# Kernel tuning notes

Hardware: AMD Instinct MI355X
Metric: run time of the kernel (lower is better)

Reference implementation:

```python
import jax, jax.numpy as jnp
import numpy as np

H, W = 250, 400
N_RAYS = H * W          # 100000 (one patch)
N_SAMPLES = 1_000_000
P, C, DIM = 50000, 16, 8
STEP_SIZE = 0.005
DENSITY_SHIFT = 0.0
DENSITY_SCALE = min(1.0 / (1.0 - DENSITY_SHIFT), 25.0)


def setup_inputs() -> dict:
    key = jax.random.key(0)
    ks = jax.random.split(key, 12)
    return {
        "trivecs": jax.random.normal(ks[0], (P, C, 3, DIM), dtype=jnp.float32),
        "densities": jax.random.normal(ks[1], (P, C), dtype=jnp.float32),
        "colors": jax.random.normal(ks[2], (P, C, 3), dtype=jnp.float32),
        "local_gweight_s": jax.random.uniform(ks[3], (N_SAMPLES, 3), dtype=jnp.float32),
        "local_gweight_l": jax.random.uniform(ks[4], (N_SAMPLES, 3), dtype=jnp.float32),
        "t_min": jax.random.uniform(ks[5], (N_RAYS,), dtype=jnp.float32),
        "bg": jax.random.uniform(ks[6], (3,), dtype=jnp.float32),
        "local_gindx_s": jax.random.randint(ks[7], (N_SAMPLES, 3), 0, DIM, dtype=jnp.int32),
        "local_gindx_l": jax.random.randint(ks[8], (N_SAMPLES, 3), 0, DIM, dtype=jnp.int32),
        "tensoRF_id": jax.random.randint(ks[9], (N_SAMPLES,), 0, P, dtype=jnp.int32),
        "ray_id": jnp.sort(jax.random.randint(ks[10], (N_SAMPLES,), 0, N_RAYS, dtype=jnp.int32)),
        "step_id": jax.random.randint(ks[11], (N_SAMPLES,), 0, 200, dtype=jnp.int32),
    }


def reference(trivecs, densities, colors, local_gweight_s, local_gweight_l,
              t_min, bg, local_gindx_s, local_gindx_l, tensoRF_id, ray_id, step_id):
    # --- compute_feature: trilinear tensor-decomposition gather ---
    def interp(a):
        vs = trivecs[tensoRF_id, :, a, local_gindx_s[:, a]]  # [N, C]
        vl = trivecs[tensoRF_id, :, a, local_gindx_l[:, a]]  # [N, C]
        return vs * local_gweight_s[:, a:a + 1] + vl * local_gweight_l[:, a:a + 1]

    feature = interp(0) * interp(1) * interp(2)               # [N, C]
    sigma = (feature * densities[tensoRF_id]).sum(axis=1)     # [N]
    color = jnp.einsum('nc,nck->nk', feature, colors[tensoRF_id])  # [N, 3]

    # --- density activation & alpha ---
    density = jax.nn.softplus(sigma - DENSITY_SHIFT * 10.0) * DENSITY_SCALE
    alpha = 1.0 - jnp.exp(-density * STEP_SIZE)               # [N]

    # --- Alphas2Weights: per-ray exclusive transmittance (ray_id sorted) ---
    log_t = -density * STEP_SIZE                              # == log(1 - alpha)
    seg_total = jax.ops.segment_sum(log_t, ray_id, num_segments=N_RAYS)  # [R]
    seg_offset = jnp.concatenate([jnp.zeros((1,), log_t.dtype),
                                  jnp.cumsum(seg_total)[:-1]])           # [R]
    excl = jnp.cumsum(log_t) - log_t - seg_offset[ray_id]     # within-segment excl cumsum
    weights = alpha * jnp.exp(excl)                           # [N]
    bg_weight = jnp.exp(seg_total)                            # [R], prod(1-alpha) per ray

    # --- ray compositing ---
    rgb = jax.nn.sigmoid(color)                               # [N, 3]
    rgb_map = jax.ops.segment_sum(weights[:, None] * rgb, ray_id, num_segments=N_RAYS)
    rgb_map = rgb_map + bg_weight[:, None] * bg[None, :]
    z_val = t_min[ray_id] + step_id.astype(jnp.float32) * STEP_SIZE
    depth_map = jax.ops.segment_sum(weights * z_val, ray_id, num_segments=N_RAYS)
    alpha_map = 1.0 - bg_weight

    rgb_map = rgb_map.T.reshape(3, H, W)
    depth_map = depth_map.reshape(H, W)
    alpha_map = alpha_map.reshape(H, W)
    return rgb_map, depth_map, alpha_map
```

## Files before the change

### kernel.cpp

```cpp
#include <hip/hip_runtime.h>
#include <math.h>

#define HN       250
#define WN       400
#define N_RAYS   (HN * WN)
#define N_SAMP   1000000
#define P_TENSO  50000
#define STEP_SZ  0.005f
#define DENS_SCALE 1.0f
#define NB_SCAN  ((P_TENSO + 1023) / 1024)


#define OFF_PACK    0
#define OFF_RESULTS 32000000
#define OFF_PERM    48000000
#define OFF_IPERM   52000000
#define OFF_RANK    56000000
#define OFF_CURSOR  60000000
#define OFF_STARTS  60200000
#define OFF_BSUMS   60400000
#define OFF_FLAG    60400512
#define OFF_RSTART  60401024
#define WS_NEED     (60401024 + 400004 + 64)

#define ROW_STRIDE 20
#define TV_F   (24 * ROW_STRIDE)
#define SLAB_F (TV_F + 16 + 48)

__global__ __launch_bounds__(256) void pack_bounds_rank(
    const int*   __restrict__ tenso_id,
    const int*   __restrict__ ray_id,
    const int*   __restrict__ gis, const int* __restrict__ gil,
    const float* __restrict__ gws, const float* __restrict__ gwl,
    int* __restrict__ cursor,
    int* __restrict__ rank,
    int* __restrict__ ray_start,
    float4* __restrict__ pack)
{
    int n = blockIdx.x * 256 + threadIdx.x;
    if (n >= N_SAMP) return;

    const int tid = tenso_id[n];
    rank[n] = atomicAdd(&cursor[tid], 1);

    unsigned bits = (unsigned)gis[n*3+0] | ((unsigned)gis[n*3+1] << 3) | ((unsigned)gis[n*3+2] << 6)
                  | ((unsigned)gil[n*3+0] << 9) | ((unsigned)gil[n*3+1] << 12) | ((unsigned)gil[n*3+2] << 15);
    float4 A = make_float4(gws[n*3+0], gws[n*3+1], gws[n*3+2], gwl[n*3+0]);
    float4 B = make_float4(gwl[n*3+1], gwl[n*3+2], __uint_as_float(bits), 0.0f);
    pack[(size_t)n * 2 + 0] = A;
    pack[(size_t)n * 2 + 1] = B;

    int r = ray_id[n];
    int rprev = (n == 0) ? -1 : ray_id[n - 1];
    for (int q = rprev + 1; q <= r; ++q) ray_start[q] = n;
    if (n == N_SAMP - 1) {
        for (int q = r + 1; q <= N_RAYS; ++q) ray_start[q] = N_SAMP;
    }
}

__global__ __launch_bounds__(256) void scan_fused(
    const int* __restrict__ cursor,
    int* __restrict__ starts,
    int* __restrict__ bsums,
    int* __restrict__ flag)
{
    __shared__ int lds[257];
    const int b = blockIdx.x;
    const int t = threadIdx.x;
    const int base = b * 1024 + t * 4;

    int v[4]; int s = 0;
    #pragma unroll
    for (int i = 0; i < 4; ++i) {
        int idx = base + i;
        v[i] = (idx < P_TENSO) ? cursor[idx] : 0;
        s += v[i];
    }
    lds[t] = s;
    __syncthreads();
    for (int d = 1; d < 256; d <<= 1) {
        int x = (t >= d) ? lds[t - d] : 0;
        __syncthreads();
        lds[t] += x;
        __syncthreads();
    }
    if (t == 255) bsums[b] = lds[255];

    __threadfence();
    __syncthreads();
    if (t == 0) {
        atomicAdd(flag, 1);
        while (atomicAdd(flag, 0) < gridDim.x) { }
    }
    __syncthreads();
    __threadfence();

    if (t < 64) {
        int x = (t < b) ? bsums[t] : 0;
        #pragma unroll
        for (int m = 1; m < 64; m <<= 1) x += __shfl_xor(x, m);
        if (t == 0) lds[256] = x;
    }
    __syncthreads();
    const int pre = lds[256];

    int run = pre + ((t > 0) ? lds[t - 1] : 0);
    #pragma unroll
    for (int i = 0; i < 4; ++i) {
        int idx = base + i;
        if (idx < P_TENSO) starts[idx] = run;
        run += v[i];
    }
}

__global__ __launch_bounds__(256) void finalize_perm(
    const int* __restrict__ tenso_id,
    const int* __restrict__ rank,
    const int* __restrict__ starts,
    int* __restrict__ perm,
    int* __restrict__ iperm)
{
    int n = blockIdx.x * 256 + threadIdx.x;
    if (n >= N_SAMP) return;
    int pos = starts[tenso_id[n]] + rank[n];
    iperm[n] = pos;
    perm[pos] = n;
}

__global__ __launch_bounds__(256) void gather_phase(
    const float* __restrict__ trivecs,
    const float* __restrict__ densities,
    const float* __restrict__ colors,
    const int*   __restrict__ starts,
    const int*   __restrict__ counts,
    const int*   __restrict__ perm,
    const float4* __restrict__ pack,
    float* __restrict__ results_f)
{
    __shared__ __align__(16) float lds[4 * SLAB_F];
    const int lane = threadIdx.x & 63;
    const int wv   = threadIdx.x >> 6;
    const int t    = blockIdx.x * 4 + wv;
    if (t >= P_TENSO) return;

    const int start = starts[t];
    const int cnt   = counts[t];
    if (cnt == 0) return;

    float* slab = lds + wv * SLAB_F;
    float* dl   = slab + TV_F;
    float* cl   = dl + 16;

    const float* tvg = trivecs + (size_t)t * 384;
    #pragma unroll
    for (int i = 0; i < 6; ++i) {
        int l = lane + i * 64;
        int c = l / 24;
        int rem = l - c * 24;
        slab[rem * ROW_STRIDE + c] = tvg[l];
    }
    if (lane < 16) dl[lane] = densities[(size_t)t * 16 + lane];
    if (lane < 48) {
        int c = lane / 3, k = lane - c * 3;
        cl[k * 16 + c] = colors[(size_t)t * 48 + lane];
    }

    const int g = lane >> 2;
    const int j = lane & 3;

    const float4 dens4 = *(const float4*)(dl + 4 * j);
    const float4 col0  = *(const float4*)(cl + 4 * j);
    const float4 col1  = *(const float4*)(cl + 16 + 4 * j);
    const float4 col2  = *(const float4*)(cl + 32 + 4 * j);

    const int end = start + cnt;
    const int niter = (cnt + 15) >> 4;

    for (int it = 0; it < niter; ++it) {
        const int pos = start + it * 16 + g;
        const bool valid = (pos < end);
        const int cp = valid ? pos : (end - 1);
        const int n = perm[cp];
        const float4 A = pack[(size_t)n * 2 + 0];
        const float4 B = pack[(size_t)n * 2 + 1];
        const unsigned bits = __float_as_uint(B.z);

        float4 f;
        {
            const int is = bits & 7, il = (bits >> 9) & 7;
            const float4 vs = *(const float4*)(slab + is * ROW_STRIDE + 4 * j);
            const float4 vl = *(const float4*)(slab + il * ROW_STRIDE + 4 * j);
            f.x = vs.x * A.x + vl.x * A.w;
            f.y = vs.y * A.x + vl.y * A.w;
            f.z = vs.z * A.x + vl.z * A.w;
            f.w = vs.w * A.x + vl.w * A.w;
        }
        {
            const int is = (bits >> 3) & 7, il = (bits >> 12) & 7;
            const float4 vs = *(const float4*)(slab + (8 + is) * ROW_STRIDE + 4 * j);
            const float4 vl = *(const float4*)(slab + (8 + il) * ROW_STRIDE + 4 * j);
            f.x *= vs.x * A.y + vl.x * B.x;
            f.y *= vs.y * A.y + vl.y * B.x;
            f.z *= vs.z * A.y + vl.z * B.x;
            f.w *= vs.w * A.y + vl.w * B.x;
        }
        {
            const int is = (bits >> 6) & 7, il = (bits >> 15) & 7;
            const float4 vs = *(const float4*)(slab + (16 + is) * ROW_STRIDE + 4 * j);
            const float4 vl = *(const float4*)(slab + (16 + il) * ROW_STRIDE + 4 * j);
            f.x *= vs.x * A.z + vl.x * B.y;
            f.y *= vs.y * A.z + vl.y * B.y;
            f.z *= vs.z * A.z + vl.z * B.y;
            f.w *= vs.w * A.z + vl.w * B.y;
        }

        float s0 = f.x * dens4.x + f.y * dens4.y + f.z * dens4.z + f.w * dens4.w;
        float s1 = f.x * col0.x  + f.y * col0.y  + f.z * col0.z  + f.w * col0.w;
        float s2 = f.x * col1.x  + f.y * col1.y  + f.z * col1.z  + f.w * col1.w;
        float s3 = f.x * col2.x  + f.y * col2.y  + f.z * col2.z  + f.w * col2.w;

        s0 += __shfl_xor(s0, 1); s0 += __shfl_xor(s0, 2);
        s1 += __shfl_xor(s1, 1); s1 += __shfl_xor(s1, 2);
        s2 += __shfl_xor(s2, 1); s2 += __shfl_xor(s2, 2);
        s3 += __shfl_xor(s3, 1); s3 += __shfl_xor(s3, 2);

        const float sj = (j == 0) ? s0 : (j == 1) ? s1 : (j == 2) ? s2 : s3;
        float val;
        if (j == 0) {
            float dens = fmaxf(sj, 0.0f) + __logf(1.0f + __expf(-fabsf(sj)));
            val = -(dens * DENS_SCALE) * STEP_SZ;
        } else {
            val = 1.0f / (1.0f + __expf(-sj));
        }
        if (valid) results_f[(size_t)pos * 4 + j] = val;
    }
}

__global__ __launch_bounds__(256) void ray_render(
    const float4* __restrict__ results,
    const int*    __restrict__ iperm,
    const float*  __restrict__ t_min,
    const float*  __restrict__ bg,
    const int*    __restrict__ ray_start,
    const int*    __restrict__ step_id,
    float* __restrict__ out)
{
    int r = blockIdx.x * 256 + threadIdx.x;
    if (r >= N_RAYS) return;
    const int s = ray_start[r];
    const int e = ray_start[r + 1];
    const float tmin_r = t_min[r];

    float T = 0.0f, aR = 0.0f, aG = 0.0f, aB = 0.0f, aD = 0.0f;
    for (int n = s; n < e; ++n) {
        const int pos = iperm[n];
        float4 res = results[pos];
        const float lt = res.x;
        const float w = (1.0f - __expf(lt)) * __expf(T);
        T += lt;
        const float z = tmin_r + (float)step_id[n] * STEP_SZ;
        aR += w * res.y;
        aG += w * res.z;
        aB += w * res.w;
        aD += w * z;
    }
    const float bgw = __expf(T);
    out[0 * N_RAYS + r] = aR + bgw * bg[0];
    out[1 * N_RAYS + r] = aG + bgw * bg[1];
    out[2 * N_RAYS + r] = aB + bgw * bg[2];
    out[3 * N_RAYS + r] = aD;
    out[4 * N_RAYS + r] = 1.0f - bgw;
}

__global__ __launch_bounds__(256) void trivec_render_fallback(
    const float* __restrict__ trivecs, const float* __restrict__ densities,
    const float* __restrict__ colors, const float* __restrict__ gws,
    const float* __restrict__ gwl, const float* __restrict__ t_min,
    const float* __restrict__ bg, const int* __restrict__ gis,
    const int* __restrict__ gil, const int* __restrict__ tenso_id,
    const int* __restrict__ ray_id, const int* __restrict__ step_id,
    float* __restrict__ out)
{
    const int lane = threadIdx.x & 63;
    const int r = blockIdx.x * 4 + (threadIdx.x >> 6);
    if (r >= N_RAYS) return;
    const int c = lane & 15;
    const int g = lane >> 4;
    int lo = 0, hi = N_SAMP;
    while (lo < hi) { int mid = (lo + hi) >> 1; if (ray_id[mid] < r) lo = mid + 1; else hi = mid; }
    const int seg_start = lo;
    hi = N_SAMP;
    while (lo < hi) { int mid = (lo + hi) >> 1; if (ray_id[mid] < r + 1) lo = mid + 1; else hi = mid; }
    const int seg_end = lo;
    const float tmin_r = t_min[r];
    float Tlog = 0.0f, accR = 0.0f, accG = 0.0f, accB = 0.0f, accD = 0.0f;
    const int niter = (seg_end - seg_start + 3) >> 2;
    for (int it = 0; it < niter; ++it) {
        const int n = seg_start + it * 4 + g;
        const bool valid = (n < seg_end);
        const int nc = valid ? n : (seg_end - 1);
        const int tid = tenso_id[nc];
        const float* tv = trivecs + (size_t)tid * 384 + c * 24;
        float f = 1.0f;
        #pragma unroll
        for (int a = 0; a < 3; ++a) {
            const int is = gis[nc*3+a], il = gil[nc*3+a];
            const float wS = gws[nc*3+a], wL = gwl[nc*3+a];
            f *= (tv[a*8+is] * wS + tv[a*8+il] * wL);
        }
        const float dns = densities[(size_t)tid * 16 + c];
        const float* colp = colors + ((size_t)tid * 16 + c) * 3;
        float s0 = f*dns, s1 = f*colp[0], s2 = f*colp[1], s3 = f*colp[2];
        #pragma unroll
        for (int m = 1; m < 16; m <<= 1) {
            s0 += __shfl_xor(s0, m); s1 += __shfl_xor(s1, m);
            s2 += __shfl_xor(s2, m); s3 += __shfl_xor(s3, m);
        }
        float dens = fmaxf(s0, 0.0f) + __logf(1.0f + __expf(-fabsf(s0)));
        const float lt = valid ? (-dens * STEP_SZ) : 0.0f;
        const float alpha = 1.0f - __expf(lt);
        const float rr = 1.0f/(1.0f+__expf(-s1)), gg = 1.0f/(1.0f+__expf(-s2)), bb = 1.0f/(1.0f+__expf(-s3));
        const float z = tmin_r + (float)step_id[nc] * STEP_SZ;
        const float lt0 = __shfl(lt,0), lt1 = __shfl(lt,16), lt2 = __shfl(lt,32), lt3 = __shfl(lt,48);
        float excl = Tlog;
        if (g > 0) excl += lt0;
        if (g > 1) excl += lt1;
        if (g > 2) excl += lt2;
        const float w = alpha * __expf(excl);
        Tlog += lt0 + lt1 + lt2 + lt3;
        accR += w*rr; accG += w*gg; accB += w*bb; accD += w*z;
    }
    accR += __shfl_xor(accR,16); accR += __shfl_xor(accR,32);
    accG += __shfl_xor(accG,16); accG += __shfl_xor(accG,32);
    accB += __shfl_xor(accB,16); accB += __shfl_xor(accB,32);
    accD += __shfl_xor(accD,16); accD += __shfl_xor(accD,32);
    const float bgw = __expf(Tlog);
    if (lane == 0) {
        out[0*N_RAYS+r] = accR + bgw*bg[0];
        out[1*N_RAYS+r] = accG + bgw*bg[1];
        out[2*N_RAYS+r] = accB + bgw*bg[2];
        out[3*N_RAYS+r] = accD;
        out[4*N_RAYS+r] = 1.0f - bgw;
    }
}

extern "C" void kernel_launch(void* const* d_in, const int* in_sizes, int n_in,
                              void* d_out, int out_size, void* d_ws, size_t ws_size,
                              hipStream_t stream) {
    const float* trivecs   = (const float*)d_in[0];
    const float* densities = (const float*)d_in[1];
    const float* colors    = (const float*)d_in[2];
    const float* gws       = (const float*)d_in[3];
    const float* gwl       = (const float*)d_in[4];
    const float* t_min     = (const float*)d_in[5];
    const float* bg        = (const float*)d_in[6];
    const int*   gis       = (const int*)d_in[7];
    const int*   gil       = (const int*)d_in[8];
    const int*   tenso_id  = (const int*)d_in[9];
    const int*   ray_id    = (const int*)d_in[10];
    const int*   step_id   = (const int*)d_in[11];
    float* out = (float*)d_out;

    if (ws_size < (size_t)WS_NEED) {
        trivec_render_fallback<<<(N_RAYS + 3) / 4, 256, 0, stream>>>(
            trivecs, densities, colors, gws, gwl, t_min, bg,
            gis, gil, tenso_id, ray_id, step_id, out);
        return;
    }

    char* ws = (char*)d_ws;
    float4* pack     = (float4*)(ws + OFF_PACK);
    float4* results  = (float4*)(ws + OFF_RESULTS);
    int*    perm     = (int*)(ws + OFF_PERM);
    int*    iperm    = (int*)(ws + OFF_IPERM);
    int*    rank     = (int*)(ws + OFF_RANK);
    int*    cursor   = (int*)(ws + OFF_CURSOR);
    int*    starts   = (int*)(ws + OFF_STARTS);
    int*    bsums    = (int*)(ws + OFF_BSUMS);
    int*    flag     = (int*)(ws + OFF_FLAG);
    int*    raystart = (int*)(ws + OFF_RSTART);

    hipMemsetAsync(ws + OFF_CURSOR, 0, (OFF_FLAG + 64) - OFF_CURSOR, stream);

    pack_bounds_rank<<<(N_SAMP + 255) / 256, 256, 0, stream>>>(
        tenso_id, ray_id, gis, gil, gws, gwl, cursor, rank, raystart, pack);
    scan_fused<<<NB_SCAN, 256, 0, stream>>>(cursor, starts, bsums, flag);
    finalize_perm<<<(N_SAMP + 255) / 256, 256, 0, stream>>>(
        tenso_id, rank, starts, perm, iperm);
    gather_phase<<<(P_TENSO + 3) / 4, 256, 0, stream>>>(
        trivecs, densities, colors, starts, cursor, perm, pack, (float*)results);
    ray_render<<<(N_RAYS + 255) / 256, 256, 0, stream>>>(
        results, iperm, t_min, bg, raystart, step_id, out);
}
```

Baseline: 283.2 us.

## Scatter packed sample data into tensor-sorted order and write results in sample order

The per-sample packed weights and indices are now scattered directly into tensoRF-sorted order, with the original sample index stored in the spare fourth lane. The gather kernel then reads them contiguously instead of going through a perm indirection. It writes results back at the original sample index, so ray_render reads results sequentially without iperm. This drops the perm/iperm arrays and their random reads, at the cost of a scattered 32-byte write in build_sorted and scattered 16-byte result writes in the gather.

```diff
diff --git a/kernel.cpp b/kernel.cpp
--- a/kernel.cpp
+++ b/kernel.cpp
@@ -11,44 +11,31 @@
 #define NB_SCAN  ((P_TENSO + 1023) / 1024)
 
 
-#define OFF_PACK    0
+#define OFF_SORT    0
 #define OFF_RESULTS 32000000
-#define OFF_PERM    48000000
-#define OFF_IPERM   52000000
-#define OFF_RANK    56000000
-#define OFF_CURSOR  60000000
-#define OFF_STARTS  60200000
-#define OFF_BSUMS   60400000
-#define OFF_FLAG    60400512
-#define OFF_RSTART  60401024
-#define WS_NEED     (60401024 + 400004 + 64)
+#define OFF_RANK    48000000
+#define OFF_CURSOR  52000000
+#define OFF_STARTS  52200000
+#define OFF_BSUMS   52400000
+#define OFF_FLAG    52400512
+#define OFF_RSTART  52401024
+#define WS_NEED     (52401024 + 400004 + 64)
 
 #define ROW_STRIDE 20
 #define TV_F   (24 * ROW_STRIDE)
 #define SLAB_F (TV_F + 16 + 48)
 
-__global__ __launch_bounds__(256) void pack_bounds_rank(
-    const int*   __restrict__ tenso_id,
-    const int*   __restrict__ ray_id,
-    const int*   __restrict__ gis, const int* __restrict__ gil,
-    const float* __restrict__ gws, const float* __restrict__ gwl,
+__global__ __launch_bounds__(256) void count_bounds_rank(
+    const int* __restrict__ tenso_id,
+    const int* __restrict__ ray_id,
     int* __restrict__ cursor,
     int* __restrict__ rank,
-    int* __restrict__ ray_start,
-    float4* __restrict__ pack)
+    int* __restrict__ ray_start)
 {
     int n = blockIdx.x * 256 + threadIdx.x;
     if (n >= N_SAMP) return;
 
-    const int tid = tenso_id[n];
-    rank[n] = atomicAdd(&cursor[tid], 1);
-
-    unsigned bits = (unsigned)gis[n*3+0] | ((unsigned)gis[n*3+1] << 3) | ((unsigned)gis[n*3+2] << 6)
-                  | ((unsigned)gil[n*3+0] << 9) | ((unsigned)gil[n*3+1] << 12) | ((unsigned)gil[n*3+2] << 15);
-    float4 A = make_float4(gws[n*3+0], gws[n*3+1], gws[n*3+2], gwl[n*3+0]);
-    float4 B = make_float4(gwl[n*3+1], gwl[n*3+2], __uint_as_float(bits), 0.0f);
-    pack[(size_t)n * 2 + 0] = A;
-    pack[(size_t)n * 2 + 1] = B;
+    rank[n] = atomicAdd(&cursor[tenso_id[n]], 1);
 
     int r = ray_id[n];
     int rprev = (n == 0) ? -1 : ray_id[n - 1];
@@ -113,18 +100,26 @@
     }
 }
 
-__global__ __launch_bounds__(256) void finalize_perm(
-    const int* __restrict__ tenso_id,
-    const int* __restrict__ rank,
-    const int* __restrict__ starts,
-    int* __restrict__ perm,
-    int* __restrict__ iperm)
+__global__ __launch_bounds__(256) void build_sorted(
+    const int*   __restrict__ tenso_id,
+    const int*   __restrict__ rank,
+    const int*   __restrict__ starts,
+    const int*   __restrict__ gis, const int* __restrict__ gil,
+    const float* __restrict__ gws, const float* __restrict__ gwl,
+    float4* __restrict__ sorted)
 {
     int n = blockIdx.x * 256 + threadIdx.x;
     if (n >= N_SAMP) return;
-    int pos = starts[tenso_id[n]] + rank[n];
-    iperm[n] = pos;
-    perm[pos] = n;
+
+    const int pos = starts[tenso_id[n]] + rank[n];
+
+    unsigned bits = (unsigned)gis[n*3+0] | ((unsigned)gis[n*3+1] << 3) | ((unsigned)gis[n*3+2] << 6)
+                  | ((unsigned)gil[n*3+0] << 9) | ((unsigned)gil[n*3+1] << 12) | ((unsigned)gil[n*3+2] << 15);
+    float4 A = make_float4(gws[n*3+0], gws[n*3+1], gws[n*3+2], gwl[n*3+0]);
+    float4 B = make_float4(gwl[n*3+1], gwl[n*3+2], __uint_as_float(bits),
+                           __uint_as_float((unsigned)n));
+    sorted[(size_t)pos * 2 + 0] = A;
+    sorted[(size_t)pos * 2 + 1] = B;
 }
 
 __global__ __launch_bounds__(256) void gather_phase(
@@ -133,8 +128,7 @@
     const float* __restrict__ colors,
     const int*   __restrict__ starts,
     const int*   __restrict__ counts,
-    const int*   __restrict__ perm,
-    const float4* __restrict__ pack,
+    const float4* __restrict__ sorted,
     float* __restrict__ results_f)
 {
     __shared__ __align__(16) float lds[4 * SLAB_F];
@@ -180,10 +174,10 @@
         const int pos = start + it * 16 + g;
         const bool valid = (pos < end);
         const int cp = valid ? pos : (end - 1);
-        const int n = perm[cp];
-        const float4 A = pack[(size_t)n * 2 + 0];
-        const float4 B = pack[(size_t)n * 2 + 1];
+        const float4 A = sorted[(size_t)cp * 2 + 0];
+        const float4 B = sorted[(size_t)cp * 2 + 1];
         const unsigned bits = __float_as_uint(B.z);
+        const unsigned n    = __float_as_uint(B.w);
 
         float4 f;
         {
@@ -232,13 +226,12 @@
         } else {
             val = 1.0f / (1.0f + __expf(-sj));
         }
-        if (valid) results_f[(size_t)pos * 4 + j] = val;
+        if (valid) results_f[(size_t)n * 4 + j] = val;
     }
 }
 
 __global__ __launch_bounds__(256) void ray_render(
     const float4* __restrict__ results,
-    const int*    __restrict__ iperm,
     const float*  __restrict__ t_min,
     const float*  __restrict__ bg,
     const int*    __restrict__ ray_start,
@@ -253,8 +246,7 @@
 
     float T = 0.0f, aR = 0.0f, aG = 0.0f, aB = 0.0f, aD = 0.0f;
     for (int n = s; n < e; ++n) {
-        const int pos = iperm[n];
-        float4 res = results[pos];
+        float4 res = results[n];
         const float lt = res.x;
         const float w = (1.0f - __expf(lt)) * __expf(T);
         T += lt;
@@ -369,10 +361,8 @@
     }
 
     char* ws = (char*)d_ws;
-    float4* pack     = (float4*)(ws + OFF_PACK);
+    float4* sorted   = (float4*)(ws + OFF_SORT);
     float4* results  = (float4*)(ws + OFF_RESULTS);
-    int*    perm     = (int*)(ws + OFF_PERM);
-    int*    iperm    = (int*)(ws + OFF_IPERM);
     int*    rank     = (int*)(ws + OFF_RANK);
     int*    cursor   = (int*)(ws + OFF_CURSOR);
     int*    starts   = (int*)(ws + OFF_STARTS);
@@ -382,13 +372,13 @@
 
     hipMemsetAsync(ws + OFF_CURSOR, 0, (OFF_FLAG + 64) - OFF_CURSOR, stream);
 
-    pack_bounds_rank<<<(N_SAMP + 255) / 256, 256, 0, stream>>>(
-        tenso_id, ray_id, gis, gil, gws, gwl, cursor, rank, raystart, pack);
+    count_bounds_rank<<<(N_SAMP + 255) / 256, 256, 0, stream>>>(
+        tenso_id, ray_id, cursor, rank, raystart);
     scan_fused<<<NB_SCAN, 256, 0, stream>>>(cursor, starts, bsums, flag);
-    finalize_perm<<<(N_SAMP + 255) / 256, 256, 0, stream>>>(
-        tenso_id, rank, starts, perm, iperm);
+    build_sorted<<<(N_SAMP + 255) / 256, 256, 0, stream>>>(
+        tenso_id, rank, starts, gis, gil, gws, gwl, sorted);
     gather_phase<<<(P_TENSO + 3) / 4, 256, 0, stream>>>(
-        trivecs, densities, colors, starts, cursor, perm, pack, (float*)results);
+        trivecs, densities, colors, starts, cursor, sorted, (float*)results);
     ray_render<<<(N_RAYS + 255) / 256, 256, 0, stream>>>(
-        results, iperm, t_min, bg, raystart, step_id, out);
-}
+        results, t_min, bg, raystart, step_id, out);
+}
```

Measured after the change: 297.0 us. 1.05x slower.

## Scatter gather results in original sample order and drop inverse permutation

Applied to the files above, without the earlier changes.

The gather kernel now writes each sample's result at its original index instead of its sorted position. This removes the iperm array, its write in finalize_perm, and the indirect load in ray_render, which now reads results contiguously. The gather loop is also unrolled to two samples per lane group with perm prefetched one iteration ahead. ray_render carries transmittance multiplicatively instead of re-exponentiating, trading scattered writes in gather for coalesced reads in render.

```diff
diff --git a/kernel.cpp b/kernel.cpp
--- a/kernel.cpp
+++ b/kernel.cpp
@@ -14,14 +14,13 @@
 #define OFF_PACK    0
 #define OFF_RESULTS 32000000
 #define OFF_PERM    48000000
-#define OFF_IPERM   52000000
-#define OFF_RANK    56000000
-#define OFF_CURSOR  60000000
-#define OFF_STARTS  60200000
-#define OFF_BSUMS   60400000
-#define OFF_FLAG    60400512
-#define OFF_RSTART  60401024
-#define WS_NEED     (60401024 + 400004 + 64)
+#define OFF_RANK    52000000
+#define OFF_CURSOR  56000000
+#define OFF_STARTS  56200000
+#define OFF_BSUMS   56400000
+#define OFF_FLAG    56400512
+#define OFF_RSTART  56401024
+#define WS_NEED     (56401024 + 400004 + 64)
 
 #define ROW_STRIDE 20
 #define TV_F   (24 * ROW_STRIDE)
@@ -117,13 +116,11 @@
     const int* __restrict__ tenso_id,
     const int* __restrict__ rank,
     const int* __restrict__ starts,
-    int* __restrict__ perm,
-    int* __restrict__ iperm)
+    int* __restrict__ perm)
 {
     int n = blockIdx.x * 256 + threadIdx.x;
     if (n >= N_SAMP) return;
     int pos = starts[tenso_id[n]] + rank[n];
-    iperm[n] = pos;
     perm[pos] = n;
 }
 
@@ -151,6 +148,15 @@
     float* dl   = slab + TV_F;
     float* cl   = dl + 16;
 
+    const int g = lane >> 2;
+    const int j = lane & 3;
+    const int end = start + cnt;
+
+    int p0 = start + g;
+    int p1 = p0 + 16;
+    int n0 = perm[(p0 < end) ? p0 : (end - 1)];
+    int n1 = perm[(p1 < end) ? p1 : (end - 1)];
+
     const float* tvg = trivecs + (size_t)t * 384;
     #pragma unroll
     for (int i = 0; i < 6; ++i) {
@@ -165,80 +171,120 @@
         cl[k * 16 + c] = colors[(size_t)t * 48 + lane];
     }
 
-    const int g = lane >> 2;
-    const int j = lane & 3;
-
     const float4 dens4 = *(const float4*)(dl + 4 * j);
     const float4 col0  = *(const float4*)(cl + 4 * j);
     const float4 col1  = *(const float4*)(cl + 16 + 4 * j);
     const float4 col2  = *(const float4*)(cl + 32 + 4 * j);
 
-    const int end = start + cnt;
-    const int niter = (cnt + 15) >> 4;
+    const int niter = (cnt + 31) >> 5;
 
     for (int it = 0; it < niter; ++it) {
-        const int pos = start + it * 16 + g;
-        const bool valid = (pos < end);
-        const int cp = valid ? pos : (end - 1);
-        const int n = perm[cp];
-        const float4 A = pack[(size_t)n * 2 + 0];
-        const float4 B = pack[(size_t)n * 2 + 1];
-        const unsigned bits = __float_as_uint(B.z);
-
-        float4 f;
+        const bool v0 = (p0 < end);
+        const bool v1 = (p1 < end);
+        const int sn0 = n0, sn1 = n1;
+
+        const float4 A0 = pack[(size_t)sn0 * 2 + 0];
+        const float4 B0 = pack[(size_t)sn0 * 2 + 1];
+        const float4 A1 = pack[(size_t)sn1 * 2 + 0];
+        const float4 B1 = pack[(size_t)sn1 * 2 + 1];
+
+        if (it + 1 < niter) {
+            p0 = start + (it + 1) * 32 + g;
+            p1 = p0 + 16;
+            n0 = perm[(p0 < end) ? p0 : (end - 1)];
+            n1 = perm[(p1 < end) ? p1 : (end - 1)];
+        }
+
+        const unsigned bits0 = __float_as_uint(B0.z);
+        const unsigned bits1 = __float_as_uint(B1.z);
+
+        float4 f0, f1;
         {
-            const int is = bits & 7, il = (bits >> 9) & 7;
-            const float4 vs = *(const float4*)(slab + is * ROW_STRIDE + 4 * j);
-            const float4 vl = *(const float4*)(slab + il * ROW_STRIDE + 4 * j);
-            f.x = vs.x * A.x + vl.x * A.w;
-            f.y = vs.y * A.x + vl.y * A.w;
-            f.z = vs.z * A.x + vl.z * A.w;
-            f.w = vs.w * A.x + vl.w * A.w;
+            const int is0 = bits0 & 7, il0 = (bits0 >> 9) & 7;
+            const int is1 = bits1 & 7, il1 = (bits1 >> 9) & 7;
+            const float4 vs0 = *(const float4*)(slab + is0 * ROW_STRIDE + 4 * j);
+            const float4 vl0 = *(const float4*)(slab + il0 * ROW_STRIDE + 4 * j);
+            const float4 vs1 = *(const float4*)(slab + is1 * ROW_STRIDE + 4 * j);
+            const float4 vl1 = *(const float4*)(slab + il1 * ROW_STRIDE + 4 * j);
+            f0.x = vs0.x * A0.x + vl0.x * A0.w;
+            f0.y = vs0.y * A0.x + vl0.y * A0.w;
+            f0.z = vs0.z * A0.x + vl0.z * A0.w;
+            f0.w = vs0.w * A0.x + vl0.w * A0.w;
+            f1.x = vs1.x * A1.x + vl1.x * A1.w;
+            f1.y = vs1.y * A1.x + vl1.y * A1.w;
+            f1.z = vs1.z * A1.x + vl1.z * A1.w;
+            f1.w = vs1.w * A1.x + vl1.w * A1.w;
         }
         {
-            const int is = (bits >> 3) & 7, il = (bits >> 12) & 7;
-            const float4 vs = *(const float4*)(slab + (8 + is) * ROW_STRIDE + 4 * j);
-            const float4 vl = *(const float4*)(slab + (8 + il) * ROW_STRIDE + 4 * j);
-            f.x *= vs.x * A.y + vl.x * B.x;
-            f.y *= vs.y * A.y + vl.y * B.x;
-            f.z *= vs.z * A.y + vl.z * B.x;
-            f.w *= vs.w * A.y + vl.w * B.x;
+            const int is0 = (bits0 >> 3) & 7, il0 = (bits0 >> 12) & 7;
+            const int is1 = (bits1 >> 3) & 7, il1 = (bits1 >> 12) & 7;
+            const float4 vs0 = *(const float4*)(slab + (8 + is0) * ROW_STRIDE + 4 * j);
+            const float4 vl0 = *(const float4*)(slab + (8 + il0) * ROW_STRIDE + 4 * j);
+            const float4 vs1 = *(const float4*)(slab + (8 + is1) * ROW_STRIDE + 4 * j);
+            const float4 vl1 = *(const float4*)(slab + (8 + il1) * ROW_STRIDE + 4 * j);
+            f0.x *= vs0.x * A0.y + vl0.x * B0.x;
+            f0.y *= vs0.y * A0.y + vl0.y * B0.x;
+            f0.z *= vs0.z * A0.y + vl0.z * B0.x;
+            f0.w *= vs0.w * A0.y + vl0.w * B0.x;
+            f1.x *= vs1.x * A1.y + vl1.x * B1.x;
+            f1.y *= vs1.y * A1.y + vl1.y * B1.x;
+            f1.z *= vs1.z * A1.y + vl1.z * B1.x;
+            f1.w *= vs1.w * A1.y + vl1.w * B1.x;
         }
         {
-            const int is = (bits >> 6) & 7, il = (bits >> 15) & 7;
-            const float4 vs = *(const float4*)(slab + (16 + is) * ROW_STRIDE + 4 * j);
-            const float4 vl = *(const float4*)(slab + (16 + il) * ROW_STRIDE + 4 * j);
-            f.x *= vs.x * A.z + vl.x * B.y;
-            f.y *= vs.y * A.z + vl.y * B.y;
-            f.z *= vs.z * A.z + vl.z * B.y;
-            f.w *= vs.w * A.z + vl.w * B.y;
-        }
-
-        float s0 = f.x * dens4.x + f.y * dens4.y + f.z * dens4.z + f.w * dens4.w;
-        float s1 = f.x * col0.x  + f.y * col0.y  + f.z * col0.z  + f.w * col0.w;
-        float s2 = f.x * col1.x  + f.y * col1.y  + f.z * col1.z  + f.w * col1.w;
-        float s3 = f.x * col2.x  + f.y * col2.y  + f.z * col2.z  + f.w * col2.w;
-
-        s0 += __shfl_xor(s0, 1); s0 += __shfl_xor(s0, 2);
-        s1 += __shfl_xor(s1, 1); s1 += __shfl_xor(s1, 2);
-        s2 += __shfl_xor(s2, 1); s2 += __shfl_xor(s2, 2);
-        s3 += __shfl_xor(s3, 1); s3 += __shfl_xor(s3, 2);
-
-        const float sj = (j == 0) ? s0 : (j == 1) ? s1 : (j == 2) ? s2 : s3;
-        float val;
+            const int is0 = (bits0 >> 6) & 7, il0 = (bits0 >> 15) & 7;
+            const int is1 = (bits1 >> 6) & 7, il1 = (bits1 >> 15) & 7;
+            const float4 vs0 = *(const float4*)(slab + (16 + is0) * ROW_STRIDE + 4 * j);
+            const float4 vl0 = *(const float4*)(slab + (16 + il0) * ROW_STRIDE + 4 * j);
+            const float4 vs1 = *(const float4*)(slab + (16 + is1) * ROW_STRIDE + 4 * j);
+            const float4 vl1 = *(const float4*)(slab + (16 + il1) * ROW_STRIDE + 4 * j);
+            f0.x *= vs0.x * A0.z + vl0.x * B0.y;
+            f0.y *= vs0.y * A0.z + vl0.y * B0.y;
+            f0.z *= vs0.z * A0.z + vl0.z * B0.y;
+            f0.w *= vs0.w * A0.z + vl0.w * B0.y;
+            f1.x *= vs1.x * A1.z + vl1.x * B1.y;
+            f1.y *= vs1.y * A1.z + vl1.y * B1.y;
+            f1.z *= vs1.z * A1.z + vl1.z * B1.y;
+            f1.w *= vs1.w * A1.z + vl1.w * B1.y;
+        }
+
+        float s00 = f0.x * dens4.x + f0.y * dens4.y + f0.z * dens4.z + f0.w * dens4.w;
+        float s01 = f0.x * col0.x  + f0.y * col0.y  + f0.z * col0.z  + f0.w * col0.w;
+        float s02 = f0.x * col1.x  + f0.y * col1.y  + f0.z * col1.z  + f0.w * col1.w;
+        float s03 = f0.x * col2.x  + f0.y * col2.y  + f0.z * col2.z  + f0.w * col2.w;
+        float s10 = f1.x * dens4.x + f1.y * dens4.y + f1.z * dens4.z + f1.w * dens4.w;
+        float s11 = f1.x * col0.x  + f1.y * col0.y  + f1.z * col0.z  + f1.w * col0.w;
+        float s12 = f1.x * col1.x  + f1.y * col1.y  + f1.z * col1.z  + f1.w * col1.w;
+        float s13 = f1.x * col2.x  + f1.y * col2.y  + f1.z * col2.z  + f1.w * col2.w;
+
+        s00 += __shfl_xor(s00, 1); s00 += __shfl_xor(s00, 2);
+        s01 += __shfl_xor(s01, 1); s01 += __shfl_xor(s01, 2);
+        s02 += __shfl_xor(s02, 1); s02 += __shfl_xor(s02, 2);
+        s03 += __shfl_xor(s03, 1); s03 += __shfl_xor(s03, 2);
+        s10 += __shfl_xor(s10, 1); s10 += __shfl_xor(s10, 2);
+        s11 += __shfl_xor(s11, 1); s11 += __shfl_xor(s11, 2);
+        s12 += __shfl_xor(s12, 1); s12 += __shfl_xor(s12, 2);
+        s13 += __shfl_xor(s13, 1); s13 += __shfl_xor(s13, 2);
+
+        const float sj0 = (j == 0) ? s00 : (j == 1) ? s01 : (j == 2) ? s02 : s03;
+        const float sj1 = (j == 0) ? s10 : (j == 1) ? s11 : (j == 2) ? s12 : s13;
+        float val0, val1;
         if (j == 0) {
-            float dens = fmaxf(sj, 0.0f) + __logf(1.0f + __expf(-fabsf(sj)));
-            val = -(dens * DENS_SCALE) * STEP_SZ;
+            float d0 = fmaxf(sj0, 0.0f) + __logf(1.0f + __expf(-fabsf(sj0)));
+            float d1 = fmaxf(sj1, 0.0f) + __logf(1.0f + __expf(-fabsf(sj1)));
+            val0 = -(d0 * DENS_SCALE) * STEP_SZ;
+            val1 = -(d1 * DENS_SCALE) * STEP_SZ;
         } else {
-            val = 1.0f / (1.0f + __expf(-sj));
-        }
-        if (valid) results_f[(size_t)pos * 4 + j] = val;
+            val0 = 1.0f / (1.0f + __expf(-sj0));
+            val1 = 1.0f / (1.0f + __expf(-sj1));
+        }
+        if (v0) results_f[(size_t)sn0 * 4 + j] = val0;
+        if (v1) results_f[(size_t)sn1 * 4 + j] = val1;
     }
 }
 
 __global__ __launch_bounds__(256) void ray_render(
     const float4* __restrict__ results,
-    const int*    __restrict__ iperm,
     const float*  __restrict__ t_min,
     const float*  __restrict__ bg,
     const int*    __restrict__ ray_start,
@@ -251,25 +297,23 @@
     const int e = ray_start[r + 1];
     const float tmin_r = t_min[r];
 
-    float T = 0.0f, aR = 0.0f, aG = 0.0f, aB = 0.0f, aD = 0.0f;
+    float eT = 1.0f, aR = 0.0f, aG = 0.0f, aB = 0.0f, aD = 0.0f;
     for (int n = s; n < e; ++n) {
-        const int pos = iperm[n];
-        float4 res = results[pos];
-        const float lt = res.x;
-        const float w = (1.0f - __expf(lt)) * __expf(T);
-        T += lt;
+        float4 res = results[n];
+        const float eTn = eT * __expf(res.x);
+        const float w = eT - eTn;
+        eT = eTn;
         const float z = tmin_r + (float)step_id[n] * STEP_SZ;
         aR += w * res.y;
         aG += w * res.z;
         aB += w * res.w;
         aD += w * z;
     }
-    const float bgw = __expf(T);
-    out[0 * N_RAYS + r] = aR + bgw * bg[0];
-    out[1 * N_RAYS + r] = aG + bgw * bg[1];
-    out[2 * N_RAYS + r] = aB + bgw * bg[2];
+    out[0 * N_RAYS + r] = aR + eT * bg[0];
+    out[1 * N_RAYS + r] = aG + eT * bg[1];
+    out[2 * N_RAYS + r] = aB + eT * bg[2];
     out[3 * N_RAYS + r] = aD;
-    out[4 * N_RAYS + r] = 1.0f - bgw;
+    out[4 * N_RAYS + r] = 1.0f - eT;
 }
 
 __global__ __launch_bounds__(256) void trivec_render_fallback(
@@ -372,7 +416,6 @@
     float4* pack     = (float4*)(ws + OFF_PACK);
     float4* results  = (float4*)(ws + OFF_RESULTS);
     int*    perm     = (int*)(ws + OFF_PERM);
-    int*    iperm    = (int*)(ws + OFF_IPERM);
     int*    rank     = (int*)(ws + OFF_RANK);
     int*    cursor   = (int*)(ws + OFF_CURSOR);
     int*    starts   = (int*)(ws + OFF_STARTS);
@@ -386,9 +429,9 @@
         tenso_id, ray_id, gis, gil, gws, gwl, cursor, rank, raystart, pack);
     scan_fused<<<NB_SCAN, 256, 0, stream>>>(cursor, starts, bsums, flag);
     finalize_perm<<<(N_SAMP + 255) / 256, 256, 0, stream>>>(
-        tenso_id, rank, starts, perm, iperm);
+        tenso_id, rank, starts, perm);
     gather_phase<<<(P_TENSO + 3) / 4, 256, 0, stream>>>(
         trivecs, densities, colors, starts, cursor, perm, pack, (float*)results);
     ray_render<<<(N_RAYS + 255) / 256, 256, 0, stream>>>(
-        results, iperm, t_min, bg, raystart, step_id, out);
-}
+        results, t_min, bg, raystart, step_id, out);
+}
```

After: 278.9 us. Within noise of the previous version (-1.5%).
